# Kernel tuning notes

Measured on AMD Instinct MI355X. Metric: run time of the kernel, lower is better.

The kernel has to match this reference:

```python
import jax, jax.numpy as jnp
import numpy as np
import math

HEAD = 4
B, N, C = 8, 1024, 256


def setup_inputs() -> dict:
    key = jax.random.key(0)
    k1, k2, k3, k4, k5 = jax.random.split(key, 5)
    query = jax.random.normal(k1, (B, N, C), dtype=jnp.float32)
    keyt = jax.random.normal(k2, (B, N, C), dtype=jnp.float32)
    value = jax.random.normal(k3, (B, N, C), dtype=jnp.float32)
    mask = jax.random.randint(k4, (B, N, N), 0, 2).astype(bool)
    dis = jax.random.normal(k5, (B, N, N), dtype=jnp.float32)
    return {"query": query, "key": keyt, "value": value, "mask": mask, "dis": dis}


def reference(query, key, value, mask, dis):
    Bq, Nq, Cq = key.shape
    d = Cq // HEAD
    # split heads: [B,N,C] -> [h,B,N,d]
    q = query.reshape(Bq, Nq, HEAD, d).transpose(2, 0, 1, 3)
    k = key.reshape(Bq, Nq, HEAD, d).transpose(2, 0, 1, 3)
    v = value.reshape(Bq, Nq, HEAD, d).transpose(2, 0, 1, 3)
    # scores: [h,B,N,N]; note: dis added BEFORE scaling, as in the torch code
    scores = jnp.einsum('hbnd,hbmd->hbnm', q, k)
    scores = scores + dis[None]            # dis broadcasts over head dim
    scores = scores / math.sqrt(d)
    scores = jnp.where(mask[None], -jnp.inf, scores)
    p_attn = jax.nn.softmax(scores, axis=-1)
    out = jnp.einsum('hbnm,hbmd->hbnd', p_attn, v)  # [h,B,N,d]
    out = out.transpose(1, 2, 0, 3).reshape(Bq, Nq, Cq)
    return out, p_attn
```

## Files before the change

kernel.cpp:

```cpp
#include <hip/hip_runtime.h>
#include <math.h>

#define HEADS 4
#define BATCH 8
#define SEQ   1024
#define CH    256
#define DH    64
#define RB    16
#define NTHR  512
#define SSTR  1032

typedef float  floatx4  __attribute__((ext_vector_type(4)));
typedef short  shortx8  __attribute__((ext_vector_type(8)));
typedef unsigned short ushortx4 __attribute__((ext_vector_type(4)));

__device__ __forceinline__ unsigned short f2bf(float f) {
    unsigned u = __float_as_uint(f);
    unsigned r = u + 0x7FFFu + ((u >> 16) & 1u);
    return (unsigned short)(r >> 16);
}
__device__ __forceinline__ float bf2f(unsigned short h) {
    return __uint_as_float(((unsigned)h) << 16);
}
__device__ __forceinline__ shortx8 pack8(float4 a, float4 b) {
    shortx8 r;
    r[0] = (short)f2bf(a.x); r[1] = (short)f2bf(a.y);
    r[2] = (short)f2bf(a.z); r[3] = (short)f2bf(a.w);
    r[4] = (short)f2bf(b.x); r[5] = (short)f2bf(b.y);
    r[6] = (short)f2bf(b.z); r[7] = (short)f2bf(b.w);
    return r;
}

__global__ __launch_bounds__(NTHR, 8)
void attn_mfma(const float* __restrict__ q, const float* __restrict__ k,
               const float* __restrict__ v, const void* __restrict__ maskp,
               const float* __restrict__ dis, float* __restrict__ out,
               float* __restrict__ pout)
{
    __shared__ unsigned short Sraw[RB][SSTR];
    __shared__ float Opart[RB][65];
    __shared__ float part[8][RB];
    __shared__ float invs[RB];

    const int t   = threadIdx.x;
    const int bid = blockIdx.x;
    const int nb  = bid & 63;
    const int hb  = bid >> 6;
    const int b   = hb & (BATCH - 1);
    const int h   = hb >> 3;
    const int n0  = nb * RB;

    const int lane = t & 63;
    const int w    = t >> 6;
    const int ln   = lane & 15;
    const int qd   = lane >> 4;

    int fl;
    {
        const unsigned* mw = (const unsigned*)maskp;
        int found = 0;
        #pragma unroll
        for (int j = 0; j < 16; ++j)
            if (mw[lane * 16 + j] & 0xFFFFFF00u) found = 1;
        fl = (__ballot(found != 0) != 0ULL) ? 1 : 0;
    }
    const unsigned char* mask8  = (const unsigned char*)maskp;
    const int*           mask32 = (const int*)maskp;

    {
        const float* disrow = dis + ((size_t)(b * SEQ + n0)) * SEQ;
        const unsigned char* m8r  = mask8  + ((size_t)(b * SEQ + n0)) * SEQ;
        const int*           m32r = mask32 + ((size_t)(b * SEQ + n0)) * SEQ;
        #pragma unroll
        for (int i = 0; i < 8; ++i) {
            const int idx = t + NTHR * i;
            const int row = idx >> 8, c4 = (idx & 255) * 4;
            float4 dv4 = *(const float4*)(disrow + (size_t)row * SEQ + c4);
            unsigned mkb;
            if (fl) {
                mkb = *(const unsigned*)(m8r + (size_t)row * SEQ + c4);
            } else {
                int4 mv = *(const int4*)(m32r + (size_t)row * SEQ + c4);
                mkb = (mv.x ? 1u : 0u) | (mv.y ? 0x100u : 0u)
                    | (mv.z ? 0x10000u : 0u) | (mv.w ? 0x1000000u : 0u);
            }
            ushortx4 o;
            o[0] = (mkb & 0x000000FFu) ? 0xFF80u : f2bf(dv4.x);
            o[1] = (mkb & 0x0000FF00u) ? 0xFF80u : f2bf(dv4.y);
            o[2] = (mkb & 0x00FF0000u) ? 0xFF80u : f2bf(dv4.z);
            o[3] = (mkb & 0xFF000000u) ? 0xFF80u : f2bf(dv4.w);
            *(ushortx4*)&Sraw[row][c4] = o;
        }
    }

    const float* qrow = q + ((size_t)(b * SEQ + n0 + ln)) * CH + h * DH;
    shortx8 aq0, aq1;
    {
        float4 a0 = *(const float4*)(qrow + qd * 8);
        float4 a1 = *(const float4*)(qrow + qd * 8 + 4);
        float4 a2 = *(const float4*)(qrow + 32 + qd * 8);
        float4 a3 = *(const float4*)(qrow + 32 + qd * 8 + 4);
        aq0 = pack8(a0, a1);
        aq1 = pack8(a2, a3);
    }
    __syncthreads();

    const float* kbase = k + ((size_t)(b * SEQ)) * CH + h * DH;
    const float* vbase = v + ((size_t)(b * SEQ)) * CH + h * DH;

    float psum[4] = {0.f, 0.f, 0.f, 0.f};
    for (int mc = 0; mc < 8; ++mc) {
        const int mg = mc * 128 + w * 16 + ln;
        const float* krow = kbase + (size_t)mg * CH;
        float4 k0 = *(const float4*)(krow + qd * 8);
        float4 k1 = *(const float4*)(krow + qd * 8 + 4);
        float4 k2 = *(const float4*)(krow + 32 + qd * 8);
        float4 k3 = *(const float4*)(krow + 32 + qd * 8 + 4);

        shortx8 b0 = pack8(k0, k1), b1 = pack8(k2, k3);
        floatx4 acc = {0.f, 0.f, 0.f, 0.f};
        acc = __builtin_amdgcn_mfma_f32_16x16x32_bf16(aq0, b0, acc, 0, 0, 0);
        acc = __builtin_amdgcn_mfma_f32_16x16x32_bf16(aq1, b1, acc, 0, 0, 0);
        #pragma unroll
        for (int r = 0; r < 4; ++r) {
            float pre = bf2f(Sraw[qd * 4 + r][mg]);
            float ex  = __expf((acc[r] + pre) * 0.125f);
            psum[r] += ex;
            Sraw[qd * 4 + r][mg] = f2bf(ex);
        }
    }
    #pragma unroll
    for (int r = 0; r < 4; ++r) {
        float s = psum[r];
        #pragma unroll
        for (int m = 8; m; m >>= 1) s += __shfl_xor(s, m, 16);
        if (ln == 0) part[w][qd * 4 + r] = s;
    }
    __syncthreads();

    if (t < RB) {
        float s = 0.f;
        #pragma unroll
        for (int j = 0; j < 8; ++j) s += part[j][t];
        invs[t] = 1.0f / s;
    }
    __syncthreads();

    {
        float* prow = pout + ((size_t)((h * BATCH + b) * SEQ + n0)) * SEQ;
        #pragma unroll
        for (int i = 0; i < 8; ++i) {
            const int idx = t + NTHR * i;
            const int row = idx >> 8, c4 = (idx & 255) * 4;
            ushortx4 sp = *(const ushortx4*)&Sraw[row][c4];
            const float inv = invs[row];
            float4 pv = { bf2f(sp[0]) * inv, bf2f(sp[1]) * inv,
                          bf2f(sp[2]) * inv, bf2f(sp[3]) * inv };
            *(float4*)(prow + (size_t)row * SEQ + c4) = pv;
        }
    }

    const int hm = w >> 2;
    const int c  = (w & 3) * 16;
    floatx4 acco = {0.f, 0.f, 0.f, 0.f};
    for (int mc = 0; mc < 8; ++mc) {
        #pragma unroll
        for (int s = 0; s < 2; ++s) {
            const int kb = hm * 512 + mc * 64 + s * 32 + qd * 8;
            float vv[8];
            #pragma unroll
            for (int j = 0; j < 8; ++j)
                vv[j] = vbase[(size_t)(kb + j) * CH + c + ln];
            shortx8 af = *(const shortx8*)&Sraw[ln][kb];
            shortx8 bfv;
            #pragma unroll
            for (int j = 0; j < 8; ++j) bfv[j] = (short)f2bf(vv[j]);
            acco = __builtin_amdgcn_mfma_f32_16x16x32_bf16(af, bfv, acco, 0, 0, 0);
        }
    }
    if (hm == 1) {
        #pragma unroll
        for (int r = 0; r < 4; ++r) Opart[qd * 4 + r][c + ln] = acco[r];
    }
    __syncthreads();
    if (hm == 0) {
        #pragma unroll
        for (int r = 0; r < 4; ++r) {
            int row = qd * 4 + r;
            out[((size_t)(b * SEQ + n0 + row)) * CH + h * DH + c + ln]
                = (acco[r] + Opart[row][c + ln]) * invs[row];
        }
    }
}

extern "C" void kernel_launch(void* const* d_in, const int* in_sizes, int n_in,
                              void* d_out, int out_size, void* d_ws, size_t ws_size,
                              hipStream_t stream) {
    const float* q    = (const float*)d_in[0];
    const float* k    = (const float*)d_in[1];
    const float* v    = (const float*)d_in[2];
    const void*  mask = d_in[3];
    const float* dis  = (const float*)d_in[4];
    float* out  = (float*)d_out;
    float* pout = out + (size_t)BATCH * SEQ * CH;
    (void)d_ws; (void)ws_size;

    attn_mfma<<<HEADS * BATCH * (SEQ / RB), NTHR, 0, stream>>>(
        q, k, v, mask, dis, out, pout);
}
```

Measured before the change: 313.7 us.

## Stream dis/mask tiles through double-buffered LDS and interleave P stores with PV MFMA

The up-front load of the whole 16x1024 dis/mask block into LDS is replaced by a double-buffered 16x128 staging tile. Each chunk's dis/mask loads are prefetched during the QK^T MFMA of the previous chunk, with a block barrier per chunk. The p_attn global store loop is folded into the PV MFMA loop so the float2 writes overlap the V loads. The aim is to hide global latency behind compute, at the cost of extra LDS, eight more barriers, and a lower occupancy hint (6 instead of 8 blocks per CU).

```diff
diff --git a/kernel.cpp b/kernel.cpp
--- a/kernel.cpp
+++ b/kernel.cpp
@@ -9,6 +9,7 @@
 #define RB    16
 #define NTHR  512
 #define SSTR  1032
+#define PSTR  132
 
 typedef float  floatx4  __attribute__((ext_vector_type(4)));
 typedef short  shortx8  __attribute__((ext_vector_type(8)));
@@ -31,13 +32,14 @@
     return r;
 }
 
-__global__ __launch_bounds__(NTHR, 8)
+__global__ __launch_bounds__(NTHR, 6)
 void attn_mfma(const float* __restrict__ q, const float* __restrict__ k,
                const float* __restrict__ v, const void* __restrict__ maskp,
                const float* __restrict__ dis, float* __restrict__ out,
                float* __restrict__ pout)
 {
     __shared__ unsigned short Sraw[RB][SSTR];
+    __shared__ unsigned short pre[2][RB][PSTR];
     __shared__ float Opart[RB][65];
     __shared__ float part[8][RB];
     __shared__ float invs[RB];
@@ -55,6 +57,9 @@
     const int ln   = lane & 15;
     const int qd   = lane >> 4;
 
+    const int lr = t >> 5;
+    const int lc = t & 31;
+
     int fl;
     {
         const unsigned* mw = (const unsigned*)maskp;
@@ -67,31 +72,9 @@
     const unsigned char* mask8  = (const unsigned char*)maskp;
     const int*           mask32 = (const int*)maskp;
 
-    {
-        const float* disrow = dis + ((size_t)(b * SEQ + n0)) * SEQ;
-        const unsigned char* m8r  = mask8  + ((size_t)(b * SEQ + n0)) * SEQ;
-        const int*           m32r = mask32 + ((size_t)(b * SEQ + n0)) * SEQ;
-        #pragma unroll
-        for (int i = 0; i < 8; ++i) {
-            const int idx = t + NTHR * i;
-            const int row = idx >> 8, c4 = (idx & 255) * 4;
-            float4 dv4 = *(const float4*)(disrow + (size_t)row * SEQ + c4);
-            unsigned mkb;
-            if (fl) {
-                mkb = *(const unsigned*)(m8r + (size_t)row * SEQ + c4);
-            } else {
-                int4 mv = *(const int4*)(m32r + (size_t)row * SEQ + c4);
-                mkb = (mv.x ? 1u : 0u) | (mv.y ? 0x100u : 0u)
-                    | (mv.z ? 0x10000u : 0u) | (mv.w ? 0x1000000u : 0u);
-            }
-            ushortx4 o;
-            o[0] = (mkb & 0x000000FFu) ? 0xFF80u : f2bf(dv4.x);
-            o[1] = (mkb & 0x0000FF00u) ? 0xFF80u : f2bf(dv4.y);
-            o[2] = (mkb & 0x00FF0000u) ? 0xFF80u : f2bf(dv4.z);
-            o[3] = (mkb & 0xFF000000u) ? 0xFF80u : f2bf(dv4.w);
-            *(ushortx4*)&Sraw[row][c4] = o;
-        }
-    }
+    const float* disrow = dis + ((size_t)(b * SEQ + n0 + lr)) * SEQ;
+    const unsigned char* m8r  = mask8  + ((size_t)(b * SEQ + n0 + lr)) * SEQ;
+    const int*           m32r = mask32 + ((size_t)(b * SEQ + n0 + lr)) * SEQ;
 
     const float* qrow = q + ((size_t)(b * SEQ + n0 + ln)) * CH + h * DH;
     shortx8 aq0, aq1;
@@ -103,6 +86,24 @@
         aq0 = pack8(a0, a1);
         aq1 = pack8(a2, a3);
     }
+
+    {
+        float4 pd = *(const float4*)(disrow + lc * 4);
+        unsigned mkb;
+        if (fl) {
+            mkb = *(const unsigned*)(m8r + lc * 4);
+        } else {
+            int4 mv = *(const int4*)(m32r + lc * 4);
+            mkb = (mv.x ? 1u : 0u) | (mv.y ? 0x100u : 0u)
+                | (mv.z ? 0x10000u : 0u) | (mv.w ? 0x1000000u : 0u);
+        }
+        ushortx4 o;
+        o[0] = (mkb & 0x000000FFu) ? 0xFF80u : f2bf(pd.x);
+        o[1] = (mkb & 0x0000FF00u) ? 0xFF80u : f2bf(pd.y);
+        o[2] = (mkb & 0x00FF0000u) ? 0xFF80u : f2bf(pd.z);
+        o[3] = (mkb & 0xFF000000u) ? 0xFF80u : f2bf(pd.w);
+        *(ushortx4*)&pre[0][lr][lc * 4] = o;
+    }
     __syncthreads();
 
     const float* kbase = k + ((size_t)(b * SEQ)) * CH + h * DH;
@@ -110,25 +111,46 @@
 
     float psum[4] = {0.f, 0.f, 0.f, 0.f};
     for (int mc = 0; mc < 8; ++mc) {
+        float4 pdn; unsigned pmn = 0; int4 pm32n;
+        const int cb = (mc + 1) * 128 + lc * 4;
+        if (mc < 7) {
+            pdn = *(const float4*)(disrow + cb);
+            if (fl) pmn = *(const unsigned*)(m8r + cb);
+            else    pm32n = *(const int4*)(m32r + cb);
+        }
         const int mg = mc * 128 + w * 16 + ln;
         const float* krow = kbase + (size_t)mg * CH;
         float4 k0 = *(const float4*)(krow + qd * 8);
         float4 k1 = *(const float4*)(krow + qd * 8 + 4);
         float4 k2 = *(const float4*)(krow + 32 + qd * 8);
         float4 k3 = *(const float4*)(krow + 32 + qd * 8 + 4);
-
         shortx8 b0 = pack8(k0, k1), b1 = pack8(k2, k3);
         floatx4 acc = {0.f, 0.f, 0.f, 0.f};
         acc = __builtin_amdgcn_mfma_f32_16x16x32_bf16(aq0, b0, acc, 0, 0, 0);
         acc = __builtin_amdgcn_mfma_f32_16x16x32_bf16(aq1, b1, acc, 0, 0, 0);
+        const int colw = w * 16 + ln;
         #pragma unroll
         for (int r = 0; r < 4; ++r) {
-            float pre = bf2f(Sraw[qd * 4 + r][mg]);
-            float ex  = __expf((acc[r] + pre) * 0.125f);
+            float pv = bf2f(pre[mc & 1][qd * 4 + r][colw]);
+            float ex = __expf((acc[r] + pv) * 0.125f);
             psum[r] += ex;
             Sraw[qd * 4 + r][mg] = f2bf(ex);
         }
-    }
+        if (mc < 7) {
+            unsigned mkb;
+            if (fl) mkb = pmn;
+            else mkb = (pm32n.x ? 1u : 0u) | (pm32n.y ? 0x100u : 0u)
+                     | (pm32n.z ? 0x10000u : 0u) | (pm32n.w ? 0x1000000u : 0u);
+            ushortx4 o;
+            o[0] = (mkb & 0x000000FFu) ? 0xFF80u : f2bf(pdn.x);
+            o[1] = (mkb & 0x0000FF00u) ? 0xFF80u : f2bf(pdn.y);
+            o[2] = (mkb & 0x00FF0000u) ? 0xFF80u : f2bf(pdn.z);
+            o[3] = (mkb & 0xFF000000u) ? 0xFF80u : f2bf(pdn.w);
+            *(ushortx4*)&pre[(mc + 1) & 1][lr][lc * 4] = o;
+        }
+        __syncthreads();
+    }
+
     #pragma unroll
     for (int r = 0; r < 4; ++r) {
         float s = psum[r];
@@ -146,37 +168,28 @@
     }
     __syncthreads();
 
-    {
-        float* prow = pout + ((size_t)((h * BATCH + b) * SEQ + n0)) * SEQ;
-        #pragma unroll
-        for (int i = 0; i < 8; ++i) {
-            const int idx = t + NTHR * i;
-            const int row = idx >> 8, c4 = (idx & 255) * 4;
-            ushortx4 sp = *(const ushortx4*)&Sraw[row][c4];
-            const float inv = invs[row];
-            float4 pv = { bf2f(sp[0]) * inv, bf2f(sp[1]) * inv,
-                          bf2f(sp[2]) * inv, bf2f(sp[3]) * inv };
-            *(float4*)(prow + (size_t)row * SEQ + c4) = pv;
-        }
-    }
-
     const int hm = w >> 2;
     const int c  = (w & 3) * 16;
+    float* prow = pout + ((size_t)((h * BATCH + b) * SEQ + n0)) * SEQ;
     floatx4 acco = {0.f, 0.f, 0.f, 0.f};
-    for (int mc = 0; mc < 8; ++mc) {
-        #pragma unroll
-        for (int s = 0; s < 2; ++s) {
-            const int kb = hm * 512 + mc * 64 + s * 32 + qd * 8;
-            float vv[8];
-            #pragma unroll
-            for (int j = 0; j < 8; ++j)
-                vv[j] = vbase[(size_t)(kb + j) * CH + c + ln];
-            shortx8 af = *(const shortx8*)&Sraw[ln][kb];
-            shortx8 bfv;
-            #pragma unroll
-            for (int j = 0; j < 8; ++j) bfv[j] = (short)f2bf(vv[j]);
-            acco = __builtin_amdgcn_mfma_f32_16x16x32_bf16(af, bfv, acco, 0, 0, 0);
-        }
+    for (int st = 0; st < 16; ++st) {
+        const int kb = hm * 512 + st * 32 + qd * 8;
+        float vv[8];
+        #pragma unroll
+        for (int j = 0; j < 8; ++j)
+            vv[j] = vbase[(size_t)(kb + j) * CH + c + ln];
+        {
+            const float inv = invs[st];
+            unsigned pk = *(const unsigned*)&Sraw[st][t * 2];
+            float2 pv = { bf2f((unsigned short)(pk & 0xFFFFu)) * inv,
+                          bf2f((unsigned short)(pk >> 16)) * inv };
+            *(float2*)(prow + (size_t)st * SEQ + t * 2) = pv;
+        }
+        shortx8 af = *(const shortx8*)&Sraw[ln][kb];
+        shortx8 bfv;
+        #pragma unroll
+        for (int j = 0; j < 8; ++j) bfv[j] = (short)f2bf(vv[j]);
+        acco = __builtin_amdgcn_mfma_f32_16x16x32_bf16(af, bfv, acco, 0, 0, 0);
     }
     if (hm == 1) {
         #pragma unroll
```

After: 318.7 us. About the same (+1.6%).
